# Kernel optimization log

Hardware: AMD Instinct MI355X
Metric: run time of the kernel (lower is better)

The kernel has to match this reference:

```python
import jax, jax.numpy as jnp
import numpy as np

DIM, N_HEAD, N_KV, HEAD_DIM = 2048, 16, 4, 128
ROPE_BASE = 10000.0
ROPE_FACTOR = 1.0  # YaRN with factor=1 == plain RoPE


def setup_inputs() -> dict:
    key = jax.random.key(0)
    k1, k2, k3, k4 = jax.random.split(key, 4)
    b, s = 4, 2048
    sc = 1.0 / np.sqrt(DIM)
    return {
        "x": jax.random.normal(k1, (b, s, DIM), dtype=jnp.float32),
        "Wq": jax.random.normal(k2, (DIM, DIM), dtype=jnp.float32) * sc,
        "Wkv": jax.random.normal(k3, (2 * N_KV * HEAD_DIM, DIM), dtype=jnp.float32) * sc,
        "Wo": jax.random.normal(k4, (DIM, DIM), dtype=jnp.float32) * sc,
    }


def _rope_cos_sin(seqlen, start_pos=0):
    inv_freq = 1.0 / (ROPE_BASE ** (jnp.arange(0, HEAD_DIM, 2, dtype=jnp.float32) / HEAD_DIM))
    pos = (jnp.arange(seqlen, dtype=jnp.float32) + start_pos) / ROPE_FACTOR
    ang = pos[:, None] * inv_freq  # (s, hd/2)
    cos = jnp.concatenate([jnp.cos(ang), jnp.cos(ang)], axis=-1)  # (s, hd)
    sin = jnp.concatenate([jnp.sin(ang), jnp.sin(ang)], axis=-1)
    return cos[None, :, None, :], sin[None, :, None, :]  # (1, s, 1, hd)


def _rotate_half(t):
    h = HEAD_DIM // 2
    return jnp.concatenate([-t[..., h:], t[..., :h]], axis=-1)


def reference(x, Wq, Wkv, Wo):
    b, s, dim = x.shape
    G = N_HEAD // N_KV  # query heads per kv head
    q = (x @ Wq.T).reshape(b, s, N_HEAD, HEAD_DIM)                 # (b,s,H,hd)
    kv = (x @ Wkv.T).reshape(b, s, 2, N_KV, HEAD_DIM)
    k, v = kv[:, :, 0], kv[:, :, 1]                                # (b,s,KV,hd)
    cos, sin = _rope_cos_sin(s)
    q = q * cos + _rotate_half(q) * sin
    k = k * cos + _rotate_half(k) * sin
    # grouped attention: head h attends kv head h // G (matches repeat_interleave)
    qg = q.transpose(0, 2, 1, 3).reshape(b, N_KV, G, s, HEAD_DIM)  # (b,KV,G,s,hd)
    kt = k.transpose(0, 2, 1, 3)                                   # (b,KV,s,hd)
    vt = v.transpose(0, 2, 1, 3)
    scale = 1.0 / jnp.sqrt(jnp.asarray(HEAD_DIM, dtype=x.dtype))
    scores = jnp.einsum('bkgqd,bkpd->bkgqp', qg, kt) * scale       # (b,KV,G,s,s)
    causal = jnp.tril(jnp.ones((s, s), dtype=bool))
    scores = jnp.where(causal, scores, jnp.asarray(-jnp.inf, dtype=scores.dtype))
    probs = jax.nn.softmax(scores, axis=-1)
    out = jnp.einsum('bkgqp,bkpd->bkgqd', probs, vt)               # (b,KV,G,s,hd)
    out = out.reshape(b, N_HEAD, s, HEAD_DIM).transpose(0, 2, 1, 3).reshape(b, s, dim)
    return out @ Wo.T
```

## Files before the change

kernel.cpp:

```cpp
#include <hip/hip_runtime.h>
#include <hip/hip_bf16.h>

typedef __hip_bfloat16 bf16;
typedef __attribute__((ext_vector_type(4))) float f32x4;
typedef __attribute__((ext_vector_type(16))) float f32x16;
typedef __attribute__((ext_vector_type(8))) short short8;
typedef __attribute__((ext_vector_type(4))) unsigned u32x4;

#define NHEAD 16
#define NKV 4
#define HD 128
#define BATCH 4
#define SEQ 2048
#define DIMM 2048
#define NROWS (BATCH*SEQ)
#define QKVN (DIMM + 2*NKV*HD)

__device__ inline void gload_lds16(const bf16* g, bf16* l) {
  __builtin_amdgcn_global_load_lds(
      (const __attribute__((address_space(1))) unsigned int*)g,
      (__attribute__((address_space(3))) unsigned int*)l, 16, 0, 0);
}

__device__ inline unsigned cvtpk(float a, float b) {
  unsigned r;
  asm("v_cvt_pk_bf16_f32 %0, %1, %2" : "=v"(r) : "v"(a), "v"(b));
  return r;
}
__device__ inline void pswap(unsigned& x, unsigned& y) {
  asm volatile("v_permlane32_swap_b32 %0, %1" : "+v"(x), "+v"(y));
}

__global__ void cvt_f32_bf16(const float* __restrict__ s, bf16* __restrict__ d, int n) {
  for (int i = (blockIdx.x * blockDim.x + threadIdx.x) * 4; i < n;
       i += gridDim.x * blockDim.x * 4) {
    const float4 v = *reinterpret_cast<const float4*>(s + i);
    alignas(8) bf16 t[4] = {__float2bfloat16(v.x), __float2bfloat16(v.y),
                            __float2bfloat16(v.z), __float2bfloat16(v.w)};
    *reinterpret_cast<uint2*>(d + i) = *reinterpret_cast<const uint2*>(t);
  }
}

__device__ inline void store_c(float* p, float v) { *p = v; }
__device__ inline void store_c(bf16* p, float v) { *p = __float2bfloat16(v); }

template <typename OutT>
__global__ __launch_bounds__(512, 2) void gemm256(
    const bf16* __restrict__ A, const bf16* __restrict__ B0,
    const bf16* __restrict__ B1, OutT* __restrict__ C,
    int M, int N, int K, int Nsplit) {
  __shared__ __align__(16) short As[2][2][256 * 32];
  __shared__ __align__(16) short Bs[2][2][256 * 32];
  const int tid = threadIdx.x;
  const int w = tid >> 6, l = tid & 63;
  const int m0 = blockIdx.x * 256, n0 = blockIdx.y * 256;
  const bf16* Ap = A + (size_t)m0 * K;
  const bf16* Bp = (n0 < Nsplit) ? (B0 + (size_t)n0 * K)
                                 : (B1 + (size_t)(n0 - Nsplit) * K);
  const int wr = w >> 2, wc = w & 3;
  const int lr = l & 15, lc = l >> 4;
  const int swz = lc ^ (l & 3) ^ ((l >> 2) & 1);

  f32x4 acc[8][4] = {};
  const int KT = K >> 6;

  auto stage = [&](int kt, int kh, int buf) {
#pragma unroll
    for (int j = 0; j < 2; ++j) {
      const int cbase = j * 512 + w * 64;
      const int ch = cbase + l;
      const int row = ch >> 2, c = ch & 3;
      const int sc = c ^ (row & 3) ^ ((row >> 2) & 1);
      const int gcol = kt * 64 + kh * 32 + sc * 8;
      gload_lds16(Ap + (size_t)row * K + gcol, (bf16*)&As[buf][kh][cbase * 8]);
      gload_lds16(Bp + (size_t)row * K + gcol, (bf16*)&Bs[buf][kh][cbase * 8]);
    }
  };

  stage(0, 0, 0);
  stage(0, 1, 0);
  stage(1, 0, 1);

  for (int kt = 0; kt < KT; ++kt) {
    const int cur = kt & 1;
#pragma unroll
    for (int kh = 0; kh < 2; ++kh) {
      if (kt < KT - 1) {
        asm volatile("s_waitcnt vmcnt(8)" ::: "memory");
      } else if (kh == 0) {
        asm volatile("s_waitcnt vmcnt(4)" ::: "memory");
      } else {
        asm volatile("s_waitcnt vmcnt(0)" ::: "memory");
      }
      __builtin_amdgcn_s_barrier();
      __builtin_amdgcn_sched_barrier(0);

      short8 a[8], b[4];
      const short* Ab = &As[cur][kh][0];
      const short* Bb = &Bs[cur][kh][0];
#pragma unroll
      for (int mr = 0; mr < 8; ++mr)
        a[mr] = *(const short8*)&Ab[(wr * 128 + mr * 16 + lr) * 32 + swz * 8];
#pragma unroll
      for (int nr = 0; nr < 4; ++nr)
        b[nr] = *(const short8*)&Bb[(wc * 64 + nr * 16 + lr) * 32 + swz * 8];

      {
        const int g = 2 * kt + kh + 3;
        const int st = g >> 1;
        if (st < KT) stage(st, g & 1, st & 1);
      }

      asm volatile("s_waitcnt lgkmcnt(0)" ::: "memory");
      __builtin_amdgcn_sched_barrier(0);
      __builtin_amdgcn_s_setprio(1);
#pragma unroll
      for (int mr = 0; mr < 8; ++mr)
#pragma unroll
        for (int nr = 0; nr < 4; ++nr)
          acc[mr][nr] = __builtin_amdgcn_mfma_f32_16x16x32_bf16(
              a[mr], b[nr], acc[mr][nr], 0, 0, 0);
      __builtin_amdgcn_s_setprio(0);
    }
  }

  const int cr4 = (l >> 4) * 4;
#pragma unroll
  for (int mr = 0; mr < 8; ++mr)
#pragma unroll
    for (int nr = 0; nr < 4; ++nr)
#pragma unroll
      for (int r = 0; r < 4; ++r) {
        const int row = m0 + wr * 128 + mr * 16 + cr4 + r;
        const int col = n0 + wc * 64 + nr * 16 + lr;
        store_c(&C[(size_t)row * N + col], acc[mr][nr][r]);
      }
}

__global__ void rope_kernel(bf16* __restrict__ qkv) {
  const int idx = blockIdx.x * blockDim.x + threadIdx.x;
  const int total = NROWS * 20 * 64;
  if (idx >= total) return;
  const int d = idx & 63;
  const int slot = (idx >> 6) % 20;
  const int row = idx / (64 * 20);
  const int col = (slot < 16) ? slot * 128 : DIMM + (slot - 16) * 128;
  const size_t base = (size_t)row * QKVN + col;
  const int pos = row & (SEQ - 1);
  const float inv = exp2f((float)d * (-2.0f / 128.0f) * 13.287712379549449f);
  const float ang = (float)pos * inv;
  float sn, cs;
  __sincosf(ang, &sn, &cs);
  const float psc = (slot < 16) ? 0.12751879895f : 1.0f;
  const float lo = __bfloat162float(qkv[base + d]);
  const float hi = __bfloat162float(qkv[base + d + 64]);
  qkv[base + d] = __float2bfloat16((lo * cs - hi * sn) * psc);
  qkv[base + d + 64] = __float2bfloat16((hi * cs + lo * sn) * psc);
}

__global__ __launch_bounds__(256) void vtrans_kernel(const bf16* __restrict__ qkv,
                                                     bf16* __restrict__ vtg) {
  __shared__ short T[64 * 72];
  const int si = blockIdx.x * 64;
  const int di = blockIdx.y * 64;
  const int b = blockIdx.z >> 2, kvh = blockIdx.z & 3;
  const int t = threadIdx.x;
  const int r = t >> 2, c2 = (t & 3) * 2;
  const bf16* src =
      qkv + (size_t)(b * SEQ + si + r) * QKVN + DIMM + NKV * HD + kvh * 128 + di;
#pragma unroll
  for (int i = 0; i < 2; ++i)
    *(short8*)&T[r * 72 + (c2 + i) * 8] = *(const short8*)(src + (c2 + i) * 8);
  __syncthreads();
#pragma unroll
  for (int i = 0; i < 2; ++i) {
    short8 v;
    const int s8 = (c2 + i) * 8;
#pragma unroll
    for (int j = 0; j < 8; ++j) v[j] = T[(s8 + j) * 72 + r];
    *(short8*)(vtg + (size_t)(kvh * 128 + di + r) * NROWS + b * SEQ + si + s8) = v;
  }
}

__global__ __launch_bounds__(512, 2) void attn_kernel(
    const bf16* __restrict__ qkv, const bf16* __restrict__ vtg,
    bf16* __restrict__ aout) {
  __shared__ __align__(16) short KsL[2][64 * 128];
  __shared__ __align__(16) short VtL[2][128 * 64];
  const int tid = threadIdx.x, w = tid >> 6, l = tid & 63;
  const int lq = l & 31, hi = l >> 5;
  const int id = blockIdx.x;
  const int half = id >> 8, rr = id & 255;
  const int bh = (rr >> 3) + half * 32;
  const int j = rr & 7;
  const int qb = half ? j : 7 - j;
  const int b = bh >> 4, h = bh & 15, kvh = h >> 2;
  const int qw0 = qb * 256 + w * 32;
  const int qg = qw0 + lq;

  short8 qf[8];
  {
    const bf16* qptr = qkv + (size_t)(b * SEQ + qg) * QKVN + h * 128 + hi * 8;
#pragma unroll
    for (int s = 0; s < 8; ++s) qf[s] = *(const short8*)(qptr + s * 16);
  }

  f32x16 o[4] = {};
  float m = -1e30f, lsum = 0.f;
  const int ntiles = qb * 4 + 4;

  const bf16* Kgb = qkv + (size_t)(b * SEQ) * QKVN + DIMM + kvh * 128;
  const bf16* Vgb = vtg + (size_t)kvh * 128 * NROWS + b * SEQ;

  auto stage = [&](int kt, int buf) {
#pragma unroll
    for (int rd = 0; rd < 2; ++rd) {
      const int cb = (w * 2 + rd) * 64;
      {
        const int lc = cb + l, k = lc >> 4, c = lc & 15;
        gload_lds16(Kgb + (size_t)(kt * 64 + k) * QKVN + ((c ^ (k & 7)) * 8),
                    (bf16*)&KsL[buf][cb * 8]);
      }
      {
        const int lc = cb + l, d = lc >> 3, c = lc & 7;
        gload_lds16(Vgb + (size_t)d * NROWS + kt * 64 + ((c ^ (d & 7)) * 8),
                    (bf16*)&VtL[buf][cb * 8]);
      }
    }
  };

  stage(0, 0);
  asm volatile("s_waitcnt vmcnt(0)" ::: "memory");
  __builtin_amdgcn_s_barrier();
  __builtin_amdgcn_sched_barrier(0);

  for (int kt = 0; kt < ntiles; ++kt) {
    const int cur = kt & 1;
    if (kt + 1 < ntiles) stage(kt + 1, cur ^ 1);

    if (kt * 64 <= qw0 + 31) {
      f32x16 st[2];
#pragma unroll
      for (int ks = 0; ks < 2; ++ks) {
        const short* kb = &KsL[cur][(ks * 32 + lq) * 128];
        const int r7 = lq & 7;
        f32x16 acc = {};
#pragma unroll
        for (int s = 0; s < 8; ++s) {
          const short8 kf = *(const short8*)&kb[((2 * s + hi) ^ r7) * 8];
          acc = __builtin_amdgcn_mfma_f32_32x32x16_bf16(kf, qf[s], acc, 0, 0, 0);
        }
        st[ks] = acc;
      }
      if (kt * 64 + 63 > qw0) {
#pragma unroll
        for (int ks = 0; ks < 2; ++ks)
#pragma unroll
          for (int r = 0; r < 16; ++r) {
            const int kg = kt * 64 + ks * 32 + (r & 3) + 8 * (r >> 2) + 4 * hi;
            if (kg > qg) st[ks][r] = -1e30f;
          }
      }
      float t[16];
#pragma unroll
      for (int r = 0; r < 16; ++r) t[r] = fmaxf(st[0][r], st[1][r]);
#pragma unroll
      for (int d2 = 8; d2 > 0; d2 >>= 1)
#pragma unroll
        for (int r = 0; r < 8; ++r)
          if (r < d2) t[r] = fmaxf(t[r], t[r + d2]);
      float pm = fmaxf(t[0], __shfl_xor(t[0], 32));
      if (!__all(pm <= m + 11.0f)) {
        const float mnew = fmaxf(m, pm);
        const float fsc = __builtin_amdgcn_exp2f(m - mnew);
        m = mnew;
        lsum *= fsc;
#pragma unroll
        for (int r = 0; r < 16; ++r) {
          const float fq = __shfl(fsc, (r & 3) + 8 * (r >> 2) + 4 * hi);
#pragma unroll
          for (int db = 0; db < 4; ++db) o[db][r] *= fq;
        }
      }
      short8 pa[4];
#pragma unroll
      for (int ks = 0; ks < 2; ++ks) {
        float p[16];
        float s0 = 0.f, s1 = 0.f, s2 = 0.f, s3 = 0.f;
#pragma unroll
        for (int r = 0; r < 16; r += 4) {
          p[r] = __builtin_amdgcn_exp2f(st[ks][r] - m);         s0 += p[r];
          p[r + 1] = __builtin_amdgcn_exp2f(st[ks][r + 1] - m); s1 += p[r + 1];
          p[r + 2] = __builtin_amdgcn_exp2f(st[ks][r + 2] - m); s2 += p[r + 2];
          p[r + 3] = __builtin_amdgcn_exp2f(st[ks][r + 3] - m); s3 += p[r + 3];
        }
        lsum += (s0 + s1) + (s2 + s3);
#pragma unroll
        for (int hf = 0; hf < 2; ++hf) {
          unsigned x0 = cvtpk(p[hf * 8 + 0], p[hf * 8 + 1]);
          unsigned y0 = cvtpk(p[hf * 8 + 4], p[hf * 8 + 5]);
          unsigned x1 = cvtpk(p[hf * 8 + 2], p[hf * 8 + 3]);
          unsigned y1 = cvtpk(p[hf * 8 + 6], p[hf * 8 + 7]);
          pswap(x0, y0);
          pswap(x1, y1);
          union { u32x4 u; short8 s; } pk;
          pk.u = u32x4{x0, x1, y0, y1};
          pa[ks * 2 + hf] = pk.s;
        }
      }
#pragma unroll
      for (int s = 0; s < 4; ++s) {
        const int cc = ((2 * s + hi) ^ (lq & 7)) * 8;
#pragma unroll
        for (int db = 0; db < 4; ++db) {
          const short8 vb = *(const short8*)&VtL[cur][(db * 32 + lq) * 64 + cc];
          o[db] = __builtin_amdgcn_mfma_f32_32x32x16_bf16(pa[s], vb, o[db], 0, 0, 0);
        }
      }
    }

    asm volatile("s_waitcnt vmcnt(0)" ::: "memory");
    __builtin_amdgcn_s_barrier();
    __builtin_amdgcn_sched_barrier(0);
  }

  const float lf = lsum + __shfl_xor(lsum, 32);
#pragma unroll
  for (int r = 0; r < 16; ++r) {
    const int qr = (r & 3) + 8 * (r >> 2) + 4 * hi;
    const float linv = 1.0f / __shfl(lf, qr);
    bf16* op = aout + (size_t)(b * SEQ + qw0 + qr) * DIMM + h * 128 + lq;
#pragma unroll
    for (int db = 0; db < 4; ++db)
      op[db * 32] = __float2bfloat16(o[db][r] * linv);
  }
}

extern "C" void kernel_launch(void* const* d_in, const int* in_sizes, int n_in,
                              void* d_out, int out_size, void* d_ws, size_t ws_size,
                              hipStream_t stream) {
  const float* x = (const float*)d_in[0];
  const float* Wq = (const float*)d_in[1];
  const float* Wkv = (const float*)d_in[2];
  const float* Wo = (const float*)d_in[3];
  float* out = (float*)d_out;

  bf16* xb = (bf16*)d_ws;
  bf16* Wqb = xb + (size_t)NROWS * DIMM;
  bf16* Wkvb = Wqb + (size_t)DIMM * DIMM;
  bf16* Wob = Wkvb + (size_t)2 * NKV * HD * DIMM;
  bf16* attn = Wob + (size_t)DIMM * DIMM;
  bf16* qkv = (bf16*)d_out;
  bf16* vtg = (bf16*)d_out + (size_t)NROWS * QKVN;

  cvt_f32_bf16<<<2048, 256, 0, stream>>>(x, xb, NROWS * DIMM);
  cvt_f32_bf16<<<1024, 256, 0, stream>>>(Wq, Wqb, DIMM * DIMM);
  cvt_f32_bf16<<<512, 256, 0, stream>>>(Wkv, Wkvb, 2 * NKV * HD * DIMM);
  cvt_f32_bf16<<<1024, 256, 0, stream>>>(Wo, Wob, DIMM * DIMM);

  gemm256<bf16><<<dim3(NROWS / 256, QKVN / 256), 512, 0, stream>>>(
      xb, Wqb, Wkvb, qkv, NROWS, QKVN, DIMM, DIMM);

  rope_kernel<<<(NROWS * 20 * 64) / 256, 256, 0, stream>>>(qkv);

  vtrans_kernel<<<dim3(SEQ / 64, 2, 16), 256, 0, stream>>>(qkv, vtg);

  attn_kernel<<<dim3(512), 512, 0, stream>>>(qkv, vtg, attn);

  gemm256<float><<<dim3(NROWS / 256, DIMM / 256), 512, 0, stream>>>(
      attn, Wob, Wob, out, NROWS, DIMM, DIMM, DIMM);
}
```

Measured before the change: 327.5 us.

## Merge conversion launches, vectorize RoPE, change GEMM LDS swizzle and drop wait

```diff
diff --git a/kernel.cpp b/kernel.cpp
--- a/kernel.cpp
+++ b/kernel.cpp
@@ -30,14 +30,36 @@
 __device__ inline void pswap(unsigned& x, unsigned& y) {
   asm volatile("v_permlane32_swap_b32 %0, %1" : "+v"(x), "+v"(y));
 }
-
-__global__ void cvt_f32_bf16(const float* __restrict__ s, bf16* __restrict__ d, int n) {
-  for (int i = (blockIdx.x * blockDim.x + threadIdx.x) * 4; i < n;
-       i += gridDim.x * blockDim.x * 4) {
-    const float4 v = *reinterpret_cast<const float4*>(s + i);
+__device__ inline float bf2f(short s) {
+  return __uint_as_float(((unsigned)(unsigned short)s) << 16);
+}
+__device__ inline short f2bfbits(float f) {
+  bf16 h = __float2bfloat16(f);
+  return *reinterpret_cast<short*>(&h);
+}
+
+#define CVTN0 ((size_t)NROWS * DIMM)
+#define CVTN1 ((size_t)DIMM * DIMM)
+#define CVTN2 ((size_t)2 * NKV * HD * DIMM)
+#define CVTN3 ((size_t)DIMM * DIMM)
+__global__ void cvt_all(const float* __restrict__ x, const float* __restrict__ wq,
+                        const float* __restrict__ wkv, const float* __restrict__ wo,
+                        bf16* __restrict__ xb, bf16* __restrict__ wqb,
+                        bf16* __restrict__ wkvb, bf16* __restrict__ wob) {
+  const size_t total = CVTN0 + CVTN1 + CVTN2 + CVTN3;
+  for (size_t i = ((size_t)blockIdx.x * blockDim.x + threadIdx.x) * 4; i < total;
+       i += (size_t)gridDim.x * blockDim.x * 4) {
+    const float* s;
+    bf16* d;
+    size_t off;
+    if (i < CVTN0) { s = x; d = xb; off = i; }
+    else if (i < CVTN0 + CVTN1) { s = wq; d = wqb; off = i - CVTN0; }
+    else if (i < CVTN0 + CVTN1 + CVTN2) { s = wkv; d = wkvb; off = i - CVTN0 - CVTN1; }
+    else { s = wo; d = wob; off = i - CVTN0 - CVTN1 - CVTN2; }
+    const float4 v = *reinterpret_cast<const float4*>(s + off);
     alignas(8) bf16 t[4] = {__float2bfloat16(v.x), __float2bfloat16(v.y),
                             __float2bfloat16(v.z), __float2bfloat16(v.w)};
-    *reinterpret_cast<uint2*>(d + i) = *reinterpret_cast<const uint2*>(t);
+    *reinterpret_cast<uint2*>(d + off) = *reinterpret_cast<const uint2*>(t);
   }
 }
 
@@ -59,7 +81,7 @@
                                  : (B1 + (size_t)(n0 - Nsplit) * K);
   const int wr = w >> 2, wc = w & 3;
   const int lr = l & 15, lc = l >> 4;
-  const int swz = lc ^ (l & 3) ^ ((l >> 2) & 1);
+  const int swz = lc ^ (((lr >> 3) & 1) << 1);
 
   f32x4 acc[8][4] = {};
   const int KT = K >> 6;
@@ -70,7 +92,7 @@
       const int cbase = j * 512 + w * 64;
       const int ch = cbase + l;
       const int row = ch >> 2, c = ch & 3;
-      const int sc = c ^ (row & 3) ^ ((row >> 2) & 1);
+      const int sc = c ^ (((row >> 3) & 1) << 1);
       const int gcol = kt * 64 + kh * 32 + sc * 8;
       gload_lds16(Ap + (size_t)row * K + gcol, (bf16*)&As[buf][kh][cbase * 8]);
       gload_lds16(Bp + (size_t)row * K + gcol, (bf16*)&Bs[buf][kh][cbase * 8]);
@@ -111,8 +133,6 @@
         if (st < KT) stage(st, g & 1, st & 1);
       }
 
-      asm volatile("s_waitcnt lgkmcnt(0)" ::: "memory");
-      __builtin_amdgcn_sched_barrier(0);
       __builtin_amdgcn_s_setprio(1);
 #pragma unroll
       for (int mr = 0; mr < 8; ++mr)
@@ -139,23 +159,28 @@
 
 __global__ void rope_kernel(bf16* __restrict__ qkv) {
   const int idx = blockIdx.x * blockDim.x + threadIdx.x;
-  const int total = NROWS * 20 * 64;
-  if (idx >= total) return;
-  const int d = idx & 63;
-  const int slot = (idx >> 6) % 20;
-  const int row = idx / (64 * 20);
+  const int dc = idx & 7;
+  const int slot = (idx >> 3) % 20;
+  const int row = idx / (8 * 20);
   const int col = (slot < 16) ? slot * 128 : DIMM + (slot - 16) * 128;
   const size_t base = (size_t)row * QKVN + col;
   const int pos = row & (SEQ - 1);
-  const float inv = exp2f((float)d * (-2.0f / 128.0f) * 13.287712379549449f);
-  const float ang = (float)pos * inv;
-  float sn, cs;
-  __sincosf(ang, &sn, &cs);
   const float psc = (slot < 16) ? 0.12751879895f : 1.0f;
-  const float lo = __bfloat162float(qkv[base + d]);
-  const float hi = __bfloat162float(qkv[base + d + 64]);
-  qkv[base + d] = __float2bfloat16((lo * cs - hi * sn) * psc);
-  qkv[base + d + 64] = __float2bfloat16((hi * cs + lo * sn) * psc);
+  short8 lo = *(const short8*)(qkv + base + dc * 8);
+  short8 hi = *(const short8*)(qkv + base + 64 + dc * 8);
+  short8 olo, ohi;
+#pragma unroll
+  for (int j = 0; j < 8; ++j) {
+    const int d = dc * 8 + j;
+    const float inv = exp2f((float)d * (-2.0f / 128.0f) * 13.287712379549449f);
+    float sn, cs;
+    __sincosf((float)pos * inv, &sn, &cs);
+    const float flo = bf2f(lo[j]), fhi = bf2f(hi[j]);
+    olo[j] = f2bfbits((flo * cs - fhi * sn) * psc);
+    ohi[j] = f2bfbits((fhi * cs + flo * sn) * psc);
+  }
+  *(short8*)(qkv + base + dc * 8) = olo;
+  *(short8*)(qkv + base + 64 + dc * 8) = ohi;
 }
 
 __global__ __launch_bounds__(256) void vtrans_kernel(const bf16* __restrict__ qkv,
@@ -353,15 +378,12 @@
   bf16* qkv = (bf16*)d_out;
   bf16* vtg = (bf16*)d_out + (size_t)NROWS * QKVN;
 
-  cvt_f32_bf16<<<2048, 256, 0, stream>>>(x, xb, NROWS * DIMM);
-  cvt_f32_bf16<<<1024, 256, 0, stream>>>(Wq, Wqb, DIMM * DIMM);
-  cvt_f32_bf16<<<512, 256, 0, stream>>>(Wkv, Wkvb, 2 * NKV * HD * DIMM);
-  cvt_f32_bf16<<<1024, 256, 0, stream>>>(Wo, Wob, DIMM * DIMM);
+  cvt_all<<<2048, 256, 0, stream>>>(x, Wq, Wkv, Wo, xb, Wqb, Wkvb, Wob);
 
   gemm256<bf16><<<dim3(NROWS / 256, QKVN / 256), 512, 0, stream>>>(
       xb, Wqb, Wkvb, qkv, NROWS, QKVN, DIMM, DIMM);
 
-  rope_kernel<<<(NROWS * 20 * 64) / 256, 256, 0, stream>>>(qkv);
+  rope_kernel<<<(NROWS * 20 * 8) / 256, 256, 0, stream>>>(qkv);
 
   vtrans_kernel<<<dim3(SEQ / 64, 2, 16), 256, 0, stream>>>(qkv, vtg);
 
```

New measurement: 304.7 us. 7.0% less time.
